# Kernel optimization log

Measured on AMD Instinct MI355X. Metric: run time of the kernel, lower is better.

The kernel has to match this reference:

```python
import jax, jax.numpy as jnp
import numpy as np

T, B, C = 2048, 8, 1024
H = 8
MIN_L, MIN_R = 1, 1


def setup_inputs() -> dict:
    key = jax.random.key(0)
    k1, k2 = jax.random.split(key)
    x = jax.random.normal(k1, (T, B, C), dtype=jnp.float32)
    W_off = jax.random.normal(k2, (C, 2 * H), dtype=jnp.float32) * 0.02
    b_off = jnp.zeros((2 * H,), dtype=jnp.float32)
    return {"x": x, "W_off": W_off, "b_off": b_off}


def _interp(S, f):
    # S: (T, BH, R) cumsum; f: (T, BH) fractional index in [-1, T-1].
    # Linear interpolation of cumsum, with S(-1) == 0.
    i0 = jnp.floor(f).astype(jnp.int32)
    frac = (f - i0.astype(f.dtype))[:, :, None]
    i0c = jnp.clip(i0, 0, S.shape[0] - 1)[:, :, None]
    i1c = jnp.clip(i0 + 1, 0, S.shape[0] - 1)[:, :, None]
    v0 = jnp.where((i0 >= 0)[:, :, None], jnp.take_along_axis(S, i0c, axis=0), 0.0)
    v1 = jnp.take_along_axis(S, i1c, axis=0)
    return v0 + frac * (v1 - v0)


def reference(x, W_off, b_off):
    Tn, Bn, Cn = x.shape
    R = Cn // H
    K = MIN_L + MIN_R + 1
    # normalized cumulative sums, one lane per (batch, head)
    S = jnp.cumsum(x.reshape(Tn, Bn * H, R) * (1.0 / K), axis=0)  # (T, BH, R)
    off = jax.nn.sigmoid(x @ W_off + b_off)  # (T, B, 2H)
    aL = off[:, :, :H].reshape(Tn, Bn * H)
    aR = off[:, :, H:].reshape(Tn, Bn * H)
    t = jnp.arange(Tn, dtype=x.dtype)[:, None]  # (T, 1)
    # adaptive span lengths: minimum span plus learned fraction of max span
    lenL = MIN_L + aL * jnp.maximum(t - MIN_L, 0.0)
    lenR = MIN_R + aR * jnp.maximum((Tn - 1.0 - t) - MIN_R, 0.0)
    fL = jnp.maximum(t - lenL - 1.0, -1.0)   # left boundary - 1 (fractional)
    fR = jnp.minimum(t + lenR, Tn - 1.0)     # right boundary (fractional)
    out = _interp(S, fR) - _interp(S, fL)    # (T, BH, R)
    return out.reshape(Tn, Bn, Cn)
```

## Files before the change

### kernel.cpp

```cpp
#include <hip/hip_runtime.h>
#include <cmath>

#define T_DIM 2048
#define B_DIM 8
#define C_DIM 1024
#define H_DIM 8
#define R_DIM 128
#define BH_DIM 64
#define COLS 8192
#define COL4 2048
#define NCH 64
#define LT 32
__device__ __constant__ float INV_K = 0.33333333333333333f;

typedef _Float16 h4 __attribute__((ext_vector_type(4)));
typedef _Float16 h8 __attribute__((ext_vector_type(8)));

__global__ __launch_bounds__(256, 2) void offcsum_kernel(
        const float4* __restrict__ x4, const float* __restrict__ W,
        const float* __restrict__ bias, float* __restrict__ off,
        float4* __restrict__ csum4) {
    __shared__ float Wt[16 * 1024];
    __shared__ float sdata[4][8][64];
    const int bid = blockIdx.x;
    const int cg = bid >> 6;
    const int ch = bid & 63;
    const int tid = threadIdx.x;
    const int wave = tid >> 6, lane = tid & 63;
    const int col4 = cg * 256 + tid;

    for (int idx = tid; idx < 4096; idx += 256) {
        int c = idx >> 2, j4 = (idx & 3) * 4;
        float4 w = *reinterpret_cast<const float4*>(W + c * 16 + j4);
        Wt[(j4 + 0) * 1024 + c] = w.x;
        Wt[(j4 + 1) * 1024 + c] = w.y;
        Wt[(j4 + 2) * 1024 + c] = w.z;
        Wt[(j4 + 3) * 1024 + c] = w.w;
    }
    __syncthreads();

    const float4* xp = x4 + (size_t)(ch * LT) * COL4 + col4;
    const int cbase = tid * 4;
    float csx = 0.f, csy = 0.f, csz = 0.f, csw = 0.f;

#pragma unroll 1
    for (int g = 0; g < 8; ++g) {
        float4 xv0 = xp[(size_t)(g * 4 + 0) * COL4];
        float4 xv1 = xp[(size_t)(g * 4 + 1) * COL4];
        float4 xv2 = xp[(size_t)(g * 4 + 2) * COL4];
        float4 xv3 = xp[(size_t)(g * 4 + 3) * COL4];
        float acc[64];
#pragma unroll
        for (int i = 0; i < 64; ++i) acc[i] = 0.f;
#pragma unroll
        for (int j = 0; j < 16; ++j) {
            float4 w = *reinterpret_cast<const float4*>(&Wt[j * 1024 + cbase]);
            acc[j]      = fmaf(xv0.x, w.x, fmaf(xv0.y, w.y, fmaf(xv0.z, w.z, fmaf(xv0.w, w.w, acc[j]))));
            acc[16 + j] = fmaf(xv1.x, w.x, fmaf(xv1.y, w.y, fmaf(xv1.z, w.z, fmaf(xv1.w, w.w, acc[16 + j]))));
            acc[32 + j] = fmaf(xv2.x, w.x, fmaf(xv2.y, w.y, fmaf(xv2.z, w.z, fmaf(xv2.w, w.w, acc[32 + j]))));
            acc[48 + j] = fmaf(xv3.x, w.x, fmaf(xv3.y, w.y, fmaf(xv3.z, w.z, fmaf(xv3.w, w.w, acc[48 + j]))));
        }
        csx += xv0.x + xv1.x + xv2.x + xv3.x;
        csy += xv0.y + xv1.y + xv2.y + xv3.y;
        csz += xv0.z + xv1.z + xv2.z + xv3.z;
        csw += xv0.w + xv1.w + xv2.w + xv3.w;
#pragma unroll
        for (int m = 32; m >= 1; m >>= 1) {
            bool hi = (lane & m) != 0;
#pragma unroll
            for (int i = 0; i < m; ++i) {
                float send = hi ? acc[i] : acc[i + m];
                float recv = __shfl_xor(send, m, 64);
                acc[i] = (hi ? acc[i + m] : acc[i]) + recv;
            }
        }
        sdata[wave][g][lane] = acc[0];
    }

    float4 agg; agg.x = csx * INV_K; agg.y = csy * INV_K; agg.z = csz * INV_K; agg.w = csw * INV_K;
    csum4[(size_t)ch * COL4 + col4] = agg;

    __syncthreads();
#pragma unroll
    for (int i = 0; i < 2; ++i) {
        int idx = tid + i * 256;
        int g = idx >> 6, l = idx & 63;
        int tl = l >> 4, j = l & 15;
        float s = sdata[0][g][l] + sdata[1][g][l] + sdata[2][g][l] + sdata[3][g][l];
        s += bias[j];
        int t = ch * LT + g * 4 + tl;
        off[((size_t)t * B_DIM + cg) * 16 + j] = 1.f / (1.f + expf(-s));
    }
}

__global__ void scan_kernel(const float4* __restrict__ x4, const float4* __restrict__ csum4,
                            _Float16* __restrict__ S) {
    int gid = blockIdx.x * 256 + threadIdx.x;
    int chunk = gid >> 11;
    int col4 = gid & (COL4 - 1);
    float rx = 0.f, ry = 0.f, rz = 0.f, rw = 0.f;
    for (int c = 0; c < chunk; ++c) {
        float4 v = csum4[c * COL4 + col4];
        rx += v.x; ry += v.y; rz += v.z; rw += v.w;
    }
    const float4* xp = x4 + (size_t)chunk * LT * COL4 + col4;
    _Float16* Sp = S + (size_t)chunk * LT * COLS + col4 * 4;
#pragma unroll 4
    for (int t = 0; t < LT; ++t) {
        float4 v = xp[(size_t)t * COL4];
        rx = fmaf(v.x, INV_K, rx);
        ry = fmaf(v.y, INV_K, ry);
        rz = fmaf(v.z, INV_K, rz);
        rw = fmaf(v.w, INV_K, rw);
        h4 o; o.x = (_Float16)rx; o.y = (_Float16)ry; o.z = (_Float16)rz; o.w = (_Float16)rw;
        *reinterpret_cast<h4*>(Sp + (size_t)t * COLS) = o;
    }
}

__global__ void gather_kernel(const _Float16* __restrict__ S, const float* __restrict__ off,
                              float* __restrict__ out) {
    int bid = blockIdx.x;
    int sbid = (bid & 7) * 1024 + (bid >> 3);
    int vid = sbid * 256 + threadIdx.x;
    int r8 = (vid & 15) << 3;
    int bh = (vid >> 4) & 63;
    int t = vid >> 10;
    int b = bh >> 3, h = bh & 7;
    const float* o = off + ((size_t)t * B_DIM + b) * 16;
    float aL = o[h], aR = o[8 + h];
    float tf = (float)t;
    float lenL = 1.f + aL * fmaxf(tf - 1.f, 0.f);
    float lenR = 1.f + aR * fmaxf((float)(T_DIM - 1) - tf - 1.f, 0.f);
    float fL = fmaxf(tf - lenL - 1.f, -1.f);
    float fR = fminf(tf + lenR, (float)(T_DIM - 1));
    int col = (bh << 7) | r8;

    float ffL = floorf(fL); int i0L = (int)ffL; float frL = fL - ffL;
    float ffR = floorf(fR); int i0R = (int)ffR; float frR = fR - ffR;
    int i0Lc = min(max(i0L, 0), T_DIM - 1), i1Lc = min(i0L + 1, T_DIM - 1);
    int i0Rc = min(max(i0R, 0), T_DIM - 1), i1Rc = min(i0R + 1, T_DIM - 1);

    const h8 zero8 = {0, 0, 0, 0, 0, 0, 0, 0};
    h8 v1L = *reinterpret_cast<const h8*>(S + (size_t)i1Lc * COLS + col);
    h8 v0L = (i0L >= 0) ? *reinterpret_cast<const h8*>(S + (size_t)i0Lc * COLS + col) : zero8;
    h8 v1R = *reinterpret_cast<const h8*>(S + (size_t)i1Rc * COLS + col);
    h8 v0R = (i0R >= 0) ? *reinterpret_cast<const h8*>(S + (size_t)i0Rc * COLS + col) : zero8;

    float res[8];
#pragma unroll
    for (int i = 0; i < 8; ++i) {
        float a0 = (float)v0R[i], a1 = (float)v1R[i];
        float b0 = (float)v0L[i], b1 = (float)v1L[i];
        res[i] = fmaf(frR, a1 - a0, a0) - fmaf(frL, b1 - b0, b0);
    }
    float* op = out + (size_t)vid * 8;
    *reinterpret_cast<float4*>(op)     = make_float4(res[0], res[1], res[2], res[3]);
    *reinterpret_cast<float4*>(op + 4) = make_float4(res[4], res[5], res[6], res[7]);
}

extern "C" void kernel_launch(void* const* d_in, const int* in_sizes, int n_in,
                              void* d_out, int out_size, void* d_ws, size_t ws_size,
                              hipStream_t stream) {
    const float4* x4 = (const float4*)d_in[0];
    const float* W  = (const float*)d_in[1];
    const float* bi = (const float*)d_in[2];

    char* ws = (char*)d_ws;
    const size_t S_bytes   = (size_t)T_DIM * COLS * sizeof(_Float16);
    const size_t off_bytes = (size_t)T_DIM * B_DIM * 16 * sizeof(float);
    _Float16* S = (_Float16*)ws;
    float* off  = (float*)(ws + S_bytes);
    float* csum = (float*)(ws + S_bytes + off_bytes);

    offcsum_kernel<<<512, 256, 0, stream>>>(x4, W, bi, off, (float4*)csum);
    scan_kernel<<<(NCH * COL4) / 256, 256, 0, stream>>>(
        x4, (const float4*)csum, S);
    gather_kernel<<<(T_DIM * B_DIM * C_DIM / 8) / 256, 256, 0, stream>>>(
        S, off, (float*)d_out);
}
```

Measured before the change: 77.78 us.

## Prefetch x rows in offcsum and widen gather to 32 columns per thread

The offcsum kernel now loads the first group of x rows before the W transpose and software-prefetches the next group of four rows while computing the current one, so global load latency overlaps with the FMA work and the staging. The gather kernel switches to one block per timestep, with each thread handling 32 columns (four h8 loads per interpolation endpoint) instead of 8. This cuts the number of blocks and amortizes the per-thread offset and index math across more columns. In exchange, the prefetch and the extra gather loads raise register pressure and can lower occupancy.

```diff
diff --git a/kernel.cpp b/kernel.cpp
--- a/kernel.cpp
+++ b/kernel.cpp
@@ -29,6 +29,12 @@
     const int wave = tid >> 6, lane = tid & 63;
     const int col4 = cg * 256 + tid;
 
+    const float4* xp = x4 + (size_t)(ch * LT) * COL4 + col4;
+    float4 xv0 = xp[0];
+    float4 xv1 = xp[(size_t)1 * COL4];
+    float4 xv2 = xp[(size_t)2 * COL4];
+    float4 xv3 = xp[(size_t)3 * COL4];
+
     for (int idx = tid; idx < 4096; idx += 256) {
         int c = idx >> 2, j4 = (idx & 3) * 4;
         float4 w = *reinterpret_cast<const float4*>(W + c * 16 + j4);
@@ -39,31 +45,34 @@
     }
     __syncthreads();
 
-    const float4* xp = x4 + (size_t)(ch * LT) * COL4 + col4;
     const int cbase = tid * 4;
     float csx = 0.f, csy = 0.f, csz = 0.f, csw = 0.f;
 
 #pragma unroll 1
     for (int g = 0; g < 8; ++g) {
-        float4 xv0 = xp[(size_t)(g * 4 + 0) * COL4];
-        float4 xv1 = xp[(size_t)(g * 4 + 1) * COL4];
-        float4 xv2 = xp[(size_t)(g * 4 + 2) * COL4];
-        float4 xv3 = xp[(size_t)(g * 4 + 3) * COL4];
+        float4 c0 = xv0, c1 = xv1, c2 = xv2, c3 = xv3;
+        if (g < 7) {
+            const float4* np = xp + (size_t)((g + 1) * 4) * COL4;
+            xv0 = np[0];
+            xv1 = np[(size_t)1 * COL4];
+            xv2 = np[(size_t)2 * COL4];
+            xv3 = np[(size_t)3 * COL4];
+        }
         float acc[64];
 #pragma unroll
         for (int i = 0; i < 64; ++i) acc[i] = 0.f;
 #pragma unroll
         for (int j = 0; j < 16; ++j) {
             float4 w = *reinterpret_cast<const float4*>(&Wt[j * 1024 + cbase]);
-            acc[j]      = fmaf(xv0.x, w.x, fmaf(xv0.y, w.y, fmaf(xv0.z, w.z, fmaf(xv0.w, w.w, acc[j]))));
-            acc[16 + j] = fmaf(xv1.x, w.x, fmaf(xv1.y, w.y, fmaf(xv1.z, w.z, fmaf(xv1.w, w.w, acc[16 + j]))));
-            acc[32 + j] = fmaf(xv2.x, w.x, fmaf(xv2.y, w.y, fmaf(xv2.z, w.z, fmaf(xv2.w, w.w, acc[32 + j]))));
-            acc[48 + j] = fmaf(xv3.x, w.x, fmaf(xv3.y, w.y, fmaf(xv3.z, w.z, fmaf(xv3.w, w.w, acc[48 + j]))));
-        }
-        csx += xv0.x + xv1.x + xv2.x + xv3.x;
-        csy += xv0.y + xv1.y + xv2.y + xv3.y;
-        csz += xv0.z + xv1.z + xv2.z + xv3.z;
-        csw += xv0.w + xv1.w + xv2.w + xv3.w;
+            acc[j]      = fmaf(c0.x, w.x, fmaf(c0.y, w.y, fmaf(c0.z, w.z, fmaf(c0.w, w.w, acc[j]))));
+            acc[16 + j] = fmaf(c1.x, w.x, fmaf(c1.y, w.y, fmaf(c1.z, w.z, fmaf(c1.w, w.w, acc[16 + j]))));
+            acc[32 + j] = fmaf(c2.x, w.x, fmaf(c2.y, w.y, fmaf(c2.z, w.z, fmaf(c2.w, w.w, acc[32 + j]))));
+            acc[48 + j] = fmaf(c3.x, w.x, fmaf(c3.y, w.y, fmaf(c3.z, w.z, fmaf(c3.w, w.w, acc[48 + j]))));
+        }
+        csx += c0.x + c1.x + c2.x + c3.x;
+        csy += c0.y + c1.y + c2.y + c3.y;
+        csz += c0.z + c1.z + c2.z + c3.z;
+        csw += c0.w + c1.w + c2.w + c3.w;
 #pragma unroll
         for (int m = 32; m >= 1; m >>= 1) {
             bool hi = (lane & m) != 0;
@@ -117,14 +126,14 @@
     }
 }
 
-__global__ void gather_kernel(const _Float16* __restrict__ S, const float* __restrict__ off,
-                              float* __restrict__ out) {
+__global__ __launch_bounds__(256) void gather_kernel(
+        const _Float16* __restrict__ S, const float* __restrict__ off,
+        float* __restrict__ out) {
     int bid = blockIdx.x;
-    int sbid = (bid & 7) * 1024 + (bid >> 3);
-    int vid = sbid * 256 + threadIdx.x;
-    int r8 = (vid & 15) << 3;
-    int bh = (vid >> 4) & 63;
-    int t = vid >> 10;
+    int t = ((bid & 7) << 8) | (bid >> 3);
+    int tid = threadIdx.x;
+    int bh = tid >> 2;
+    int r32 = (tid & 3) << 5;
     int b = bh >> 3, h = bh & 7;
     const float* o = off + ((size_t)t * B_DIM + b) * 16;
     float aL = o[h], aR = o[8 + h];
@@ -133,29 +142,42 @@
     float lenR = 1.f + aR * fmaxf((float)(T_DIM - 1) - tf - 1.f, 0.f);
     float fL = fmaxf(tf - lenL - 1.f, -1.f);
     float fR = fminf(tf + lenR, (float)(T_DIM - 1));
-    int col = (bh << 7) | r8;
-
     float ffL = floorf(fL); int i0L = (int)ffL; float frL = fL - ffL;
     float ffR = floorf(fR); int i0R = (int)ffR; float frR = fR - ffR;
     int i0Lc = min(max(i0L, 0), T_DIM - 1), i1Lc = min(i0L + 1, T_DIM - 1);
     int i0Rc = min(max(i0R, 0), T_DIM - 1), i1Rc = min(i0R + 1, T_DIM - 1);
-
+    int col = (bh << 7) | r32;
+
+    const h8* p0L = reinterpret_cast<const h8*>(S + (size_t)i0Lc * COLS + col);
+    const h8* p1L = reinterpret_cast<const h8*>(S + (size_t)i1Lc * COLS + col);
+    const h8* p0R = reinterpret_cast<const h8*>(S + (size_t)i0Rc * COLS + col);
+    const h8* p1R = reinterpret_cast<const h8*>(S + (size_t)i1Rc * COLS + col);
     const h8 zero8 = {0, 0, 0, 0, 0, 0, 0, 0};
-    h8 v1L = *reinterpret_cast<const h8*>(S + (size_t)i1Lc * COLS + col);
-    h8 v0L = (i0L >= 0) ? *reinterpret_cast<const h8*>(S + (size_t)i0Lc * COLS + col) : zero8;
-    h8 v1R = *reinterpret_cast<const h8*>(S + (size_t)i1Rc * COLS + col);
-    h8 v0R = (i0R >= 0) ? *reinterpret_cast<const h8*>(S + (size_t)i0Rc * COLS + col) : zero8;
-
-    float res[8];
-#pragma unroll
-    for (int i = 0; i < 8; ++i) {
-        float a0 = (float)v0R[i], a1 = (float)v1R[i];
-        float b0 = (float)v0L[i], b1 = (float)v1L[i];
-        res[i] = fmaf(frR, a1 - a0, a0) - fmaf(frL, b1 - b0, b0);
-    }
-    float* op = out + (size_t)vid * 8;
-    *reinterpret_cast<float4*>(op)     = make_float4(res[0], res[1], res[2], res[3]);
-    *reinterpret_cast<float4*>(op + 4) = make_float4(res[4], res[5], res[6], res[7]);
+    bool mL = (i0L >= 0), mR = (i0R >= 0);
+
+    h8 a1[4], a0[4], b1[4], b0[4];
+#pragma unroll
+    for (int k = 0; k < 4; ++k) a1[k] = p1R[k];
+#pragma unroll
+    for (int k = 0; k < 4; ++k) b1[k] = p1L[k];
+#pragma unroll
+    for (int k = 0; k < 4; ++k) a0[k] = mR ? p0R[k] : zero8;
+#pragma unroll
+    for (int k = 0; k < 4; ++k) b0[k] = mL ? p0L[k] : zero8;
+
+    float* op = out + (size_t)t * COLS + col;
+#pragma unroll
+    for (int k = 0; k < 4; ++k) {
+        float r8[8];
+#pragma unroll
+        for (int i = 0; i < 8; ++i) {
+            float x0 = (float)a0[k][i], x1 = (float)a1[k][i];
+            float y0 = (float)b0[k][i], y1 = (float)b1[k][i];
+            r8[i] = fmaf(frR, x1 - x0, x0) - fmaf(frL, y1 - y0, y0);
+        }
+        *reinterpret_cast<float4*>(op + k * 8)     = make_float4(r8[0], r8[1], r8[2], r8[3]);
+        *reinterpret_cast<float4*>(op + k * 8 + 4) = make_float4(r8[4], r8[5], r8[6], r8[7]);
+    }
 }
 
 extern "C" void kernel_launch(void* const* d_in, const int* in_sizes, int n_in,
@@ -175,6 +197,5 @@
     offcsum_kernel<<<512, 256, 0, stream>>>(x4, W, bi, off, (float4*)csum);
     scan_kernel<<<(NCH * COL4) / 256, 256, 0, stream>>>(
         x4, (const float4*)csum, S);
-    gather_kernel<<<(T_DIM * B_DIM * C_DIM / 8) / 256, 256, 0, stream>>>(
-        S, off, (float*)d_out);
-}
+    gather_kernel<<<T_DIM, 256, 0, stream>>>(S, off, (float*)d_out);
+}
```

Measured after the change: 85.41 us. +9.8%, slower.

## Fuse offset projection and chunked scan into one kernel with decoupled lookback flags

Applied to the files above, without the earlier changes.

Merges the offset/chunk-sum kernel and the scan kernel into a single kernel. Each block takes a chunk index from an atomic ticket, keeps its 32 rows of x in registers, publishes its chunk sum and release flag, then spins until all earlier chunks are flagged before writing the fp16 prefix sums. This avoids re-reading x in a second kernel and removes one launch boundary. In exchange it adds a memset, spin-waiting, and heavy register pressure from holding 128 floats per thread alongside the 64 accumulators, which may cause spills.

```diff
diff --git a/kernel.cpp b/kernel.cpp
--- a/kernel.cpp
+++ b/kernel.cpp
@@ -16,18 +16,27 @@
 typedef _Float16 h4 __attribute__((ext_vector_type(4)));
 typedef _Float16 h8 __attribute__((ext_vector_type(8)));
 
-__global__ __launch_bounds__(256, 2) void offcsum_kernel(
+__global__ __launch_bounds__(256, 2) void fused_scan_kernel(
         const float4* __restrict__ x4, const float* __restrict__ W,
-        const float* __restrict__ bias, float* __restrict__ off,
-        float4* __restrict__ csum4) {
+        const float* __restrict__ bias, _Float16* __restrict__ S,
+        float* __restrict__ off, float4* __restrict__ csum4,
+        int* __restrict__ tickets, int* __restrict__ flags) {
     __shared__ float Wt[16 * 1024];
     __shared__ float sdata[4][8][64];
-    const int bid = blockIdx.x;
-    const int cg = bid >> 6;
-    const int ch = bid & 63;
+    __shared__ int s_vch;
+    const int cg = blockIdx.x >> 6;
     const int tid = threadIdx.x;
     const int wave = tid >> 6, lane = tid & 63;
+
+    if (tid == 0) s_vch = atomicAdd(&tickets[cg], 1);
+    __syncthreads();
+    const int vch = s_vch;
     const int col4 = cg * 256 + tid;
+
+    const float4* xp = x4 + (size_t)(vch * LT) * COL4 + col4;
+    float4 v[32];
+#pragma unroll
+    for (int t = 0; t < LT; ++t) v[t] = xp[(size_t)t * COL4];
 
     for (int idx = tid; idx < 4096; idx += 256) {
         int c = idx >> 2, j4 = (idx & 3) * 4;
@@ -39,31 +48,22 @@
     }
     __syncthreads();
 
-    const float4* xp = x4 + (size_t)(ch * LT) * COL4 + col4;
     const int cbase = tid * 4;
-    float csx = 0.f, csy = 0.f, csz = 0.f, csw = 0.f;
-
 #pragma unroll 1
     for (int g = 0; g < 8; ++g) {
-        float4 xv0 = xp[(size_t)(g * 4 + 0) * COL4];
-        float4 xv1 = xp[(size_t)(g * 4 + 1) * COL4];
-        float4 xv2 = xp[(size_t)(g * 4 + 2) * COL4];
-        float4 xv3 = xp[(size_t)(g * 4 + 3) * COL4];
         float acc[64];
 #pragma unroll
         for (int i = 0; i < 64; ++i) acc[i] = 0.f;
 #pragma unroll
         for (int j = 0; j < 16; ++j) {
             float4 w = *reinterpret_cast<const float4*>(&Wt[j * 1024 + cbase]);
-            acc[j]      = fmaf(xv0.x, w.x, fmaf(xv0.y, w.y, fmaf(xv0.z, w.z, fmaf(xv0.w, w.w, acc[j]))));
-            acc[16 + j] = fmaf(xv1.x, w.x, fmaf(xv1.y, w.y, fmaf(xv1.z, w.z, fmaf(xv1.w, w.w, acc[16 + j]))));
-            acc[32 + j] = fmaf(xv2.x, w.x, fmaf(xv2.y, w.y, fmaf(xv2.z, w.z, fmaf(xv2.w, w.w, acc[32 + j]))));
-            acc[48 + j] = fmaf(xv3.x, w.x, fmaf(xv3.y, w.y, fmaf(xv3.z, w.z, fmaf(xv3.w, w.w, acc[48 + j]))));
+            float4 c0 = v[g * 4 + 0], c1 = v[g * 4 + 1];
+            float4 c2 = v[g * 4 + 2], c3 = v[g * 4 + 3];
+            acc[j]      = fmaf(c0.x, w.x, fmaf(c0.y, w.y, fmaf(c0.z, w.z, fmaf(c0.w, w.w, acc[j]))));
+            acc[16 + j] = fmaf(c1.x, w.x, fmaf(c1.y, w.y, fmaf(c1.z, w.z, fmaf(c1.w, w.w, acc[16 + j]))));
+            acc[32 + j] = fmaf(c2.x, w.x, fmaf(c2.y, w.y, fmaf(c2.z, w.z, fmaf(c2.w, w.w, acc[32 + j]))));
+            acc[48 + j] = fmaf(c3.x, w.x, fmaf(c3.y, w.y, fmaf(c3.z, w.z, fmaf(c3.w, w.w, acc[48 + j]))));
         }
-        csx += xv0.x + xv1.x + xv2.x + xv3.x;
-        csy += xv0.y + xv1.y + xv2.y + xv3.y;
-        csz += xv0.z + xv1.z + xv2.z + xv3.z;
-        csw += xv0.w + xv1.w + xv2.w + xv3.w;
 #pragma unroll
         for (int m = 32; m >= 1; m >>= 1) {
             bool hi = (lane & m) != 0;
@@ -77,10 +77,19 @@
         sdata[wave][g][lane] = acc[0];
     }
 
+    float csx = 0.f, csy = 0.f, csz = 0.f, csw = 0.f;
+#pragma unroll
+    for (int t = 0; t < LT; ++t) {
+        csx += v[t].x; csy += v[t].y; csz += v[t].z; csw += v[t].w;
+    }
     float4 agg; agg.x = csx * INV_K; agg.y = csy * INV_K; agg.z = csz * INV_K; agg.w = csw * INV_K;
-    csum4[(size_t)ch * COL4 + col4] = agg;
+    csum4[(size_t)vch * COL4 + col4] = agg;
+    __threadfence();
+    __syncthreads();
+    if (tid == 0)
+        __hip_atomic_store(&flags[cg * 64 + vch], 1,
+                           __ATOMIC_RELEASE, __HIP_MEMORY_SCOPE_AGENT);
 
-    __syncthreads();
 #pragma unroll
     for (int i = 0; i < 2; ++i) {
         int idx = tid + i * 256;
@@ -88,30 +97,34 @@
         int tl = l >> 4, j = l & 15;
         float s = sdata[0][g][l] + sdata[1][g][l] + sdata[2][g][l] + sdata[3][g][l];
         s += bias[j];
-        int t = ch * LT + g * 4 + tl;
+        int t = vch * LT + g * 4 + tl;
         off[((size_t)t * B_DIM + cg) * 16 + j] = 1.f / (1.f + expf(-s));
     }
-}
 
-__global__ void scan_kernel(const float4* __restrict__ x4, const float4* __restrict__ csum4,
-                            _Float16* __restrict__ S) {
-    int gid = blockIdx.x * 256 + threadIdx.x;
-    int chunk = gid >> 11;
-    int col4 = gid & (COL4 - 1);
+    if (vch > 0) {
+        const int* fbase = flags + cg * 64;
+        while (true) {
+            int f = (lane < vch)
+                ? __hip_atomic_load(&fbase[lane], __ATOMIC_ACQUIRE, __HIP_MEMORY_SCOPE_AGENT)
+                : 1;
+            if (__all(f != 0)) break;
+            __builtin_amdgcn_s_sleep(2);
+        }
+    }
+    __threadfence();
+
     float rx = 0.f, ry = 0.f, rz = 0.f, rw = 0.f;
-    for (int c = 0; c < chunk; ++c) {
-        float4 v = csum4[c * COL4 + col4];
-        rx += v.x; ry += v.y; rz += v.z; rw += v.w;
+    for (int c = 0; c < vch; ++c) {
+        float4 p = csum4[(size_t)c * COL4 + col4];
+        rx += p.x; ry += p.y; rz += p.z; rw += p.w;
     }
-    const float4* xp = x4 + (size_t)chunk * LT * COL4 + col4;
-    _Float16* Sp = S + (size_t)chunk * LT * COLS + col4 * 4;
-#pragma unroll 4
+    _Float16* Sp = S + (size_t)(vch * LT) * COLS + col4 * 4;
+#pragma unroll
     for (int t = 0; t < LT; ++t) {
-        float4 v = xp[(size_t)t * COL4];
-        rx = fmaf(v.x, INV_K, rx);
-        ry = fmaf(v.y, INV_K, ry);
-        rz = fmaf(v.z, INV_K, rz);
-        rw = fmaf(v.w, INV_K, rw);
+        rx = fmaf(v[t].x, INV_K, rx);
+        ry = fmaf(v[t].y, INV_K, ry);
+        rz = fmaf(v[t].z, INV_K, rz);
+        rw = fmaf(v[t].w, INV_K, rw);
         h4 o; o.x = (_Float16)rx; o.y = (_Float16)ry; o.z = (_Float16)rz; o.w = (_Float16)rw;
         *reinterpret_cast<h4*>(Sp + (size_t)t * COLS) = o;
     }
@@ -166,15 +179,18 @@
     const float* bi = (const float*)d_in[2];
 
     char* ws = (char*)d_ws;
-    const size_t S_bytes   = (size_t)T_DIM * COLS * sizeof(_Float16);
-    const size_t off_bytes = (size_t)T_DIM * B_DIM * 16 * sizeof(float);
-    _Float16* S = (_Float16*)ws;
-    float* off  = (float*)(ws + S_bytes);
-    float* csum = (float*)(ws + S_bytes + off_bytes);
+    const size_t S_bytes    = (size_t)T_DIM * COLS * sizeof(_Float16);
+    const size_t off_bytes  = (size_t)T_DIM * B_DIM * 16 * sizeof(float);
+    const size_t csum_bytes = (size_t)NCH * COL4 * sizeof(float4);
+    _Float16* S  = (_Float16*)ws;
+    float* off   = (float*)(ws + S_bytes);
+    float* csum  = (float*)(ws + S_bytes + off_bytes);
+    int* tickets = (int*)(ws + S_bytes + off_bytes + csum_bytes);
+    int* flags   = tickets + 8;
 
-    offcsum_kernel<<<512, 256, 0, stream>>>(x4, W, bi, off, (float4*)csum);
-    scan_kernel<<<(NCH * COL4) / 256, 256, 0, stream>>>(
-        x4, (const float4*)csum, S);
+    hipMemsetAsync(tickets, 0, (8 + 8 * 64) * sizeof(int), stream);
+    fused_scan_kernel<<<512, 256, 0, stream>>>(x4, W, bi, S, off,
+                                               (float4*)csum, tickets, flags);
     gather_kernel<<<(T_DIM * B_DIM * C_DIM / 8) / 256, 256, 0, stream>>>(
         S, off, (float*)d_out);
 }
```

Result: slower. 295.4 us (+279.8%).

## Fuse chunk-local scan into offset kernel and add chunk prefixes in gather

Applied to the files above, without the earlier changes.

The first kernel now writes chunk-local fp16 cumulative sums while it already holds x in registers. This removes the second full read of x (64 MB) in the scan kernel. A small kernel computes per-chunk fp16 prefixes, and the gather adds the local and prefix values. In exchange the gather does twice as many loads. Precision also drops, because the prefix and the local sums are each rounded to fp16 separately.

```diff
diff --git a/kernel.cpp b/kernel.cpp
--- a/kernel.cpp
+++ b/kernel.cpp
@@ -19,7 +19,7 @@
 __global__ __launch_bounds__(256, 2) void offcsum_kernel(
         const float4* __restrict__ x4, const float* __restrict__ W,
         const float* __restrict__ bias, float* __restrict__ off,
-        float4* __restrict__ csum4) {
+        float4* __restrict__ csum4, _Float16* __restrict__ Sloc) {
     __shared__ float Wt[16 * 1024];
     __shared__ float sdata[4][8][64];
     const int bid = blockIdx.x;
@@ -40,30 +40,52 @@
     __syncthreads();
 
     const float4* xp = x4 + (size_t)(ch * LT) * COL4 + col4;
+    _Float16* Sp = Sloc + (size_t)(ch * LT) * COLS + col4 * 4;
     const int cbase = tid * 4;
     float csx = 0.f, csy = 0.f, csz = 0.f, csw = 0.f;
+    float rx = 0.f, ry = 0.f, rz = 0.f, rw = 0.f;
 
 #pragma unroll 1
     for (int g = 0; g < 8; ++g) {
-        float4 xv0 = xp[(size_t)(g * 4 + 0) * COL4];
-        float4 xv1 = xp[(size_t)(g * 4 + 1) * COL4];
-        float4 xv2 = xp[(size_t)(g * 4 + 2) * COL4];
-        float4 xv3 = xp[(size_t)(g * 4 + 3) * COL4];
+        float4 c0 = xp[(size_t)(g * 4 + 0) * COL4];
+        float4 c1 = xp[(size_t)(g * 4 + 1) * COL4];
+        float4 c2 = xp[(size_t)(g * 4 + 2) * COL4];
+        float4 c3 = xp[(size_t)(g * 4 + 3) * COL4];
         float acc[64];
 #pragma unroll
         for (int i = 0; i < 64; ++i) acc[i] = 0.f;
 #pragma unroll
         for (int j = 0; j < 16; ++j) {
             float4 w = *reinterpret_cast<const float4*>(&Wt[j * 1024 + cbase]);
-            acc[j]      = fmaf(xv0.x, w.x, fmaf(xv0.y, w.y, fmaf(xv0.z, w.z, fmaf(xv0.w, w.w, acc[j]))));
-            acc[16 + j] = fmaf(xv1.x, w.x, fmaf(xv1.y, w.y, fmaf(xv1.z, w.z, fmaf(xv1.w, w.w, acc[16 + j]))));
-            acc[32 + j] = fmaf(xv2.x, w.x, fmaf(xv2.y, w.y, fmaf(xv2.z, w.z, fmaf(xv2.w, w.w, acc[32 + j]))));
-            acc[48 + j] = fmaf(xv3.x, w.x, fmaf(xv3.y, w.y, fmaf(xv3.z, w.z, fmaf(xv3.w, w.w, acc[48 + j]))));
+            acc[j]      = fmaf(c0.x, w.x, fmaf(c0.y, w.y, fmaf(c0.z, w.z, fmaf(c0.w, w.w, acc[j]))));
+            acc[16 + j] = fmaf(c1.x, w.x, fmaf(c1.y, w.y, fmaf(c1.z, w.z, fmaf(c1.w, w.w, acc[16 + j]))));
+            acc[32 + j] = fmaf(c2.x, w.x, fmaf(c2.y, w.y, fmaf(c2.z, w.z, fmaf(c2.w, w.w, acc[32 + j]))));
+            acc[48 + j] = fmaf(c3.x, w.x, fmaf(c3.y, w.y, fmaf(c3.z, w.z, fmaf(c3.w, w.w, acc[48 + j]))));
         }
-        csx += xv0.x + xv1.x + xv2.x + xv3.x;
-        csy += xv0.y + xv1.y + xv2.y + xv3.y;
-        csz += xv0.z + xv1.z + xv2.z + xv3.z;
-        csw += xv0.w + xv1.w + xv2.w + xv3.w;
+        csx += c0.x + c1.x + c2.x + c3.x;
+        csy += c0.y + c1.y + c2.y + c3.y;
+        csz += c0.z + c1.z + c2.z + c3.z;
+        csw += c0.w + c1.w + c2.w + c3.w;
+        {
+            _Float16* sp = Sp + (size_t)(g * 4) * COLS;
+            h4 o;
+            rx = fmaf(c0.x, INV_K, rx); ry = fmaf(c0.y, INV_K, ry);
+            rz = fmaf(c0.z, INV_K, rz); rw = fmaf(c0.w, INV_K, rw);
+            o.x = (_Float16)rx; o.y = (_Float16)ry; o.z = (_Float16)rz; o.w = (_Float16)rw;
+            *reinterpret_cast<h4*>(sp) = o;
+            rx = fmaf(c1.x, INV_K, rx); ry = fmaf(c1.y, INV_K, ry);
+            rz = fmaf(c1.z, INV_K, rz); rw = fmaf(c1.w, INV_K, rw);
+            o.x = (_Float16)rx; o.y = (_Float16)ry; o.z = (_Float16)rz; o.w = (_Float16)rw;
+            *reinterpret_cast<h4*>(sp + COLS) = o;
+            rx = fmaf(c2.x, INV_K, rx); ry = fmaf(c2.y, INV_K, ry);
+            rz = fmaf(c2.z, INV_K, rz); rw = fmaf(c2.w, INV_K, rw);
+            o.x = (_Float16)rx; o.y = (_Float16)ry; o.z = (_Float16)rz; o.w = (_Float16)rw;
+            *reinterpret_cast<h4*>(sp + 2 * COLS) = o;
+            rx = fmaf(c3.x, INV_K, rx); ry = fmaf(c3.y, INV_K, ry);
+            rz = fmaf(c3.z, INV_K, rz); rw = fmaf(c3.w, INV_K, rw);
+            o.x = (_Float16)rx; o.y = (_Float16)ry; o.z = (_Float16)rz; o.w = (_Float16)rw;
+            *reinterpret_cast<h4*>(sp + 3 * COLS) = o;
+        }
 #pragma unroll
         for (int m = 32; m >= 1; m >>= 1) {
             bool hi = (lane & m) != 0;
@@ -93,31 +115,22 @@
     }
 }
 
-__global__ void scan_kernel(const float4* __restrict__ x4, const float4* __restrict__ csum4,
-                            _Float16* __restrict__ S) {
+__global__ void pfx_kernel(const float4* __restrict__ csum4, _Float16* __restrict__ pfxh) {
     int gid = blockIdx.x * 256 + threadIdx.x;
-    int chunk = gid >> 11;
+    int c = gid >> 11;
     int col4 = gid & (COL4 - 1);
     float rx = 0.f, ry = 0.f, rz = 0.f, rw = 0.f;
-    for (int c = 0; c < chunk; ++c) {
-        float4 v = csum4[c * COL4 + col4];
+    for (int k = 0; k < c; ++k) {
+        float4 v = csum4[(size_t)k * COL4 + col4];
         rx += v.x; ry += v.y; rz += v.z; rw += v.w;
     }
-    const float4* xp = x4 + (size_t)chunk * LT * COL4 + col4;
-    _Float16* Sp = S + (size_t)chunk * LT * COLS + col4 * 4;
-#pragma unroll 4
-    for (int t = 0; t < LT; ++t) {
-        float4 v = xp[(size_t)t * COL4];
-        rx = fmaf(v.x, INV_K, rx);
-        ry = fmaf(v.y, INV_K, ry);
-        rz = fmaf(v.z, INV_K, rz);
-        rw = fmaf(v.w, INV_K, rw);
-        h4 o; o.x = (_Float16)rx; o.y = (_Float16)ry; o.z = (_Float16)rz; o.w = (_Float16)rw;
-        *reinterpret_cast<h4*>(Sp + (size_t)t * COLS) = o;
-    }
-}
-
-__global__ void gather_kernel(const _Float16* __restrict__ S, const float* __restrict__ off,
+    h4 o; o.x = (_Float16)rx; o.y = (_Float16)ry; o.z = (_Float16)rz; o.w = (_Float16)rw;
+    *reinterpret_cast<h4*>(pfxh + (size_t)c * COLS + col4 * 4) = o;
+}
+
+__global__ void gather_kernel(const _Float16* __restrict__ Sloc,
+                              const _Float16* __restrict__ pfxh,
+                              const float* __restrict__ off,
                               float* __restrict__ out) {
     int bid = blockIdx.x;
     int sbid = (bid & 7) * 1024 + (bid >> 3);
@@ -141,16 +154,27 @@
     int i0Rc = min(max(i0R, 0), T_DIM - 1), i1Rc = min(i0R + 1, T_DIM - 1);
 
     const h8 zero8 = {0, 0, 0, 0, 0, 0, 0, 0};
-    h8 v1L = *reinterpret_cast<const h8*>(S + (size_t)i1Lc * COLS + col);
-    h8 v0L = (i0L >= 0) ? *reinterpret_cast<const h8*>(S + (size_t)i0Lc * COLS + col) : zero8;
-    h8 v1R = *reinterpret_cast<const h8*>(S + (size_t)i1Rc * COLS + col);
-    h8 v0R = (i0R >= 0) ? *reinterpret_cast<const h8*>(S + (size_t)i0Rc * COLS + col) : zero8;
+    h8 s1L = *reinterpret_cast<const h8*>(Sloc + (size_t)i1Lc * COLS + col);
+    h8 p1L = *reinterpret_cast<const h8*>(pfxh + (size_t)(i1Lc >> 5) * COLS + col);
+    h8 s1R = *reinterpret_cast<const h8*>(Sloc + (size_t)i1Rc * COLS + col);
+    h8 p1R = *reinterpret_cast<const h8*>(pfxh + (size_t)(i1Rc >> 5) * COLS + col);
+    h8 s0L = zero8, p0L = zero8, s0R = zero8, p0R = zero8;
+    if (i0L >= 0) {
+        s0L = *reinterpret_cast<const h8*>(Sloc + (size_t)i0Lc * COLS + col);
+        p0L = *reinterpret_cast<const h8*>(pfxh + (size_t)(i0Lc >> 5) * COLS + col);
+    }
+    if (i0R >= 0) {
+        s0R = *reinterpret_cast<const h8*>(Sloc + (size_t)i0Rc * COLS + col);
+        p0R = *reinterpret_cast<const h8*>(pfxh + (size_t)(i0Rc >> 5) * COLS + col);
+    }
 
     float res[8];
 #pragma unroll
     for (int i = 0; i < 8; ++i) {
-        float a0 = (float)v0R[i], a1 = (float)v1R[i];
-        float b0 = (float)v0L[i], b1 = (float)v1L[i];
+        float a0 = (float)s0R[i] + (float)p0R[i];
+        float a1 = (float)s1R[i] + (float)p1R[i];
+        float b0 = (float)s0L[i] + (float)p0L[i];
+        float b1 = (float)s1L[i] + (float)p1L[i];
         res[i] = fmaf(frR, a1 - a0, a0) - fmaf(frL, b1 - b0, b0);
     }
     float* op = out + (size_t)vid * 8;
@@ -166,15 +190,16 @@
     const float* bi = (const float*)d_in[2];
 
     char* ws = (char*)d_ws;
-    const size_t S_bytes   = (size_t)T_DIM * COLS * sizeof(_Float16);
-    const size_t off_bytes = (size_t)T_DIM * B_DIM * 16 * sizeof(float);
-    _Float16* S = (_Float16*)ws;
-    float* off  = (float*)(ws + S_bytes);
-    float* csum = (float*)(ws + S_bytes + off_bytes);
-
-    offcsum_kernel<<<512, 256, 0, stream>>>(x4, W, bi, off, (float4*)csum);
-    scan_kernel<<<(NCH * COL4) / 256, 256, 0, stream>>>(
-        x4, (const float4*)csum, S);
+    const size_t S_bytes    = (size_t)T_DIM * COLS * sizeof(_Float16);
+    const size_t off_bytes  = (size_t)T_DIM * B_DIM * 16 * sizeof(float);
+    const size_t csum_bytes = (size_t)NCH * COL4 * sizeof(float4);
+    _Float16* Sloc = (_Float16*)ws;
+    float* off     = (float*)(ws + S_bytes);
+    float* csum    = (float*)(ws + S_bytes + off_bytes);
+    _Float16* pfxh = (_Float16*)(ws + S_bytes + off_bytes + csum_bytes);
+
+    offcsum_kernel<<<512, 256, 0, stream>>>(x4, W, bi, off, (float4*)csum, Sloc);
+    pfx_kernel<<<(NCH * COL4) / 256, 256, 0, stream>>>((const float4*)csum, pfxh);
     gather_kernel<<<(T_DIM * B_DIM * C_DIM / 8) / 256, 256, 0, stream>>>(
-        S, off, (float*)d_out);
-}
+        Sloc, pfxh, off, (float*)d_out);
+}
```

Result: no change. 76.77 us (-1.3%).
